# Kernel optimization log

Hardware: AMD Instinct MI355X
Metric: run time of the kernel (lower is better)

Reference implementation:

```python
import jax, jax.numpy as jnp
import numpy as np

B, S, D_IN, D_OUT, H = 2, 2048, 1024, 1024, 16
DK = D_OUT // H


def setup_inputs() -> dict:
    key = jax.random.key(0)
    ks = jax.random.split(key, 6)
    s_in = 1.0 / np.sqrt(D_IN)
    s_out = 1.0 / np.sqrt(D_OUT)
    return {
        "x": jax.random.normal(ks[0], (B, S, D_IN), dtype=jnp.float32),
        "Wq": jax.random.uniform(ks[1], (D_OUT, D_IN), jnp.float32, -s_in, s_in),
        "Wk": jax.random.uniform(ks[2], (D_OUT, D_IN), jnp.float32, -s_in, s_in),
        "Wv": jax.random.uniform(ks[3], (D_OUT, D_IN), jnp.float32, -s_in, s_in),
        "Wo": jax.random.uniform(ks[4], (D_OUT, D_OUT), jnp.float32, -s_out, s_out),
        "bo": jax.random.uniform(ks[5], (D_OUT,), jnp.float32, -s_out, s_out),
    }


def reference(x, Wq, Wk, Wv, Wo, bo):
    b, s, _ = x.shape
    # torch Linear: y = x @ W.T
    q = (x @ Wq.T).reshape(b, s, H, DK).transpose(0, 2, 1, 3)  # [b,h,s,dk]
    k = (x @ Wk.T).reshape(b, s, H, DK).transpose(0, 2, 1, 3)
    v = (x @ Wv.T).reshape(b, s, H, DK).transpose(0, 2, 1, 3)
    scores = jnp.einsum("bhqd,bhkd->bhqk", q, k)
    causal = jnp.tril(jnp.ones((s, s), dtype=bool))  # True = keep
    scores = jnp.where(causal, scores, -jnp.inf)
    attn = jax.nn.softmax(scores / np.sqrt(DK), axis=-1)
    # dropout p=0.0 (eval) -> identity
    ctx = jnp.einsum("bhqk,bhkd->bhqd", attn, v)
    ctx = ctx.transpose(0, 2, 1, 3).reshape(b, s, D_OUT)
    return ctx @ Wo.T + bo
```

## Files before the change

### kernel.cpp

```cpp
#include <hip/hip_runtime.h>
#include <stdint.h>

#define B_   2
#define S_   2048
#define DIN  1024
#define DOUT 1024
#define H_   16
#define DK_  64
#define MSZ  (B_ * S_)

typedef __bf16 bf16v8 __attribute__((ext_vector_type(8)));
typedef float  f32x4  __attribute__((ext_vector_type(4)));

__device__ __forceinline__ ushort f2b(float f) {
  union { float f; uint32_t u; } a; a.f = f;
  uint32_t u = a.u;
  u += 0x7FFFu + ((u >> 16) & 1u);
  return (ushort)(u >> 16);
}

__device__ __forceinline__ uint32_t pk2(float lo, float hi) {
  union { __bf16 h; ushort u; } a, b;
  a.h = (__bf16)lo; b.h = (__bf16)hi;
  return (uint32_t)a.u | ((uint32_t)b.u << 16);
}

#define GLDS(gp, lp) __builtin_amdgcn_global_load_lds(                         \
    (const __attribute__((address_space(1))) void*)(gp),                       \
    (__attribute__((address_space(3))) void*)(lp), 16, 0, 0)

__global__ void cvt_all(const float* __restrict__ x,  const float* __restrict__ wq,
                        const float* __restrict__ wk, const float* __restrict__ wv,
                        const float* __restrict__ wo,
                        ushort* __restrict__ xb,  ushort* __restrict__ wqb,
                        ushort* __restrict__ wkb, ushort* __restrict__ wvb,
                        ushort* __restrict__ wob) {
  int i = blockIdx.x * blockDim.x + threadIdx.x;
  const int NX = 1 << 20, NW = 1 << 18;
  const float* src; ushort* dst; int off;
  if (i < NX)               { src = x;  dst = xb;  off = i; }
  else if (i < NX + NW)     { src = wq; dst = wqb; off = i - NX; }
  else if (i < NX + 2 * NW) { src = wk; dst = wkb; off = i - NX - NW; }
  else if (i < NX + 3 * NW) { src = wv; dst = wvb; off = i - NX - 2 * NW; }
  else                      { src = wo; dst = wob; off = i - NX - 3 * NW; }
  float4 v = reinterpret_cast<const float4*>(src)[off];
  ushort4 o;
  o.x = f2b(v.x); o.y = f2b(v.y); o.z = f2b(v.z); o.w = f2b(v.w);
  reinterpret_cast<ushort4*>(dst)[off] = o;
}

__global__ __launch_bounds__(256)
void gemm_qkv(const ushort* __restrict__ A,
              const ushort* __restrict__ Bq, const ushort* __restrict__ Bk,
              const ushort* __restrict__ Bv,
              ushort* __restrict__ Oq, ushort* __restrict__ Ok,
              ushort* __restrict__ Vt, int M, int K) {
  __shared__ ushort sA[128 * 64];
  __shared__ ushort sB[128 * 64];

  const int tid  = threadIdx.x;
  const int lane = tid & 63, wid = tid >> 6;
  const int wr = wid >> 1, wc = wid & 1;
  const int g = lane >> 4, c = lane & 15;
  const int m0 = blockIdx.x * 128;

  const int wsel = blockIdx.y >> 3;
  const int n0w  = (blockIdx.y & 7) * 128;
  const ushort* Bm = (wsel == 0) ? Bq : (wsel == 1) ? Bk : Bv;

  const int msk = (c & 7) << 4;

  f32x4 acc[4][4] = {};

  for (int k0 = 0; k0 < K; k0 += 64) {
    __syncthreads();
#pragma unroll
    for (int i = 0; i < 4; ++i) {
      int idx = i * 256 + tid;
      int row = idx >> 3;
      int scol = (((idx & 7) ^ (row & 7)) << 3);
      GLDS(A  + (size_t)(m0 + row) * K + k0 + scol, (char*)sA + idx * 16);
      GLDS(Bm + (size_t)(n0w + row) * K + k0 + scol, (char*)sB + idx * 16);
    }
    __syncthreads();

    bf16v8 aF[4][2], bF[4][2];
#pragma unroll
    for (int m = 0; m < 4; ++m) {
      const char* rp = (const char*)sA + (wr * 64 + m * 16 + c) * 128;
#pragma unroll
      for (int ks = 0; ks < 2; ++ks)
        aF[m][ks] = *reinterpret_cast<const bf16v8*>(rp + ((ks * 64 + g * 16) ^ msk));
    }
#pragma unroll
    for (int n = 0; n < 4; ++n) {
      const char* rp = (const char*)sB + (wc * 64 + n * 16 + c) * 128;
#pragma unroll
      for (int ks = 0; ks < 2; ++ks)
        bF[n][ks] = *reinterpret_cast<const bf16v8*>(rp + ((ks * 64 + g * 16) ^ msk));
    }
#pragma unroll
    for (int m = 0; m < 4; ++m)
#pragma unroll
      for (int n = 0; n < 4; ++n) {
        acc[m][n] = __builtin_amdgcn_mfma_f32_16x16x32_bf16(aF[m][0], bF[n][0], acc[m][n], 0, 0, 0);
        acc[m][n] = __builtin_amdgcn_mfma_f32_16x16x32_bf16(aF[m][1], bF[n][1], acc[m][n], 0, 0, 0);
      }
  }

  __syncthreads();

  if (wsel == 2) {
#pragma unroll
    for (int m = 0; m < 4; ++m)
#pragma unroll
      for (int n = 0; n < 4; ++n) {
        int row0 = m0 + wr * 64 + g * 4 + m * 16;
        int col  = n0w + wc * 64 + c + n * 16;
        int bb = row0 >> 11, ss = row0 & 2047;
        int hh = col >> 6, dd = col & 63;
        ushort4 o4;
        o4.x = f2b(acc[m][n][0]); o4.y = f2b(acc[m][n][1]);
        o4.z = f2b(acc[m][n][2]); o4.w = f2b(acc[m][n][3]);
        *reinterpret_cast<ushort4*>(
            &Vt[((size_t)(bb * 16 + hh) * 64 + dd) * 2048 + ss]) = o4;
      }
  } else {
    const float oscale = (wsel == 0) ? 0.125f * 1.4426950408889634f : 1.0f;
    ushort* Ob = (wsel == 0) ? Oq : Ok;
    char* eb = (char*)sA + wid * 2048;
#pragma unroll
    for (int m = 0; m < 4; ++m) {
#pragma unroll
      for (int n = 0; n < 4; ++n)
#pragma unroll
        for (int i = 0; i < 4; ++i) {
          int prow = g * 4 + i;
          *(ushort*)(eb + prow * 128 + ((n * 32 + c * 2) ^ ((prow & 7) << 4))) =
              f2b(acc[m][n][i] * oscale);
        }
      const int r = lane >> 2, cq = lane & 3;
      const int m2 = (r & 7) << 4;
      bf16v8 t0 = *reinterpret_cast<const bf16v8*>(eb + r * 128 + ((cq * 32) ^ m2));
      bf16v8 t1 = *reinterpret_cast<const bf16v8*>(eb + r * 128 + ((cq * 32 + 16) ^ m2));
      ushort* Gb = Ob + (size_t)(m0 + wr * 64 + m * 16 + r) * DOUT +
                   n0w + wc * 64 + cq * 16;
      *reinterpret_cast<bf16v8*>(Gb) = t0;
      *reinterpret_cast<bf16v8*>(Gb + 8) = t1;
    }
  }
}

__global__ __launch_bounds__(512)
void gemm_proj(const ushort* __restrict__ A, const ushort* __restrict__ Bw,
               float* __restrict__ Cf, const float* __restrict__ bias,
               int M, int K) {
  __shared__ char smem[32768];

  const int tid  = threadIdx.x;
  const int lane = tid & 63, wid = tid >> 6;
  const int wr = wid >> 1, wc = wid & 1;
  const int g = lane >> 4, c = lane & 15;
  const int m0 = blockIdx.x * 128, n0 = blockIdx.y * 64;

  const int msk = (c & 7) << 4;

  f32x4 acc[2][2] = {};

  for (int k0 = 0; k0 < K; k0 += 64) {
    __syncthreads();
#pragma unroll
    for (int i = 0; i < 2; ++i) {
      int idx = i * 512 + tid;
      int row = idx >> 3;
      int scol = (((idx & 7) ^ (row & 7)) << 3);
      GLDS(A + (size_t)(m0 + row) * K + k0 + scol, smem + idx * 16);
    }
    {
      int row = tid >> 3;
      int scol = (((tid & 7) ^ (row & 7)) << 3);
      GLDS(Bw + (size_t)(n0 + row) * K + k0 + scol, smem + 16384 + tid * 16);
    }
    __syncthreads();

    bf16v8 aF[2][2], bF[2][2];
#pragma unroll
    for (int m = 0; m < 2; ++m) {
      const char* rp = smem + (wr * 32 + m * 16 + c) * 128;
#pragma unroll
      for (int ks = 0; ks < 2; ++ks)
        aF[m][ks] = *reinterpret_cast<const bf16v8*>(rp + ((ks * 64 + g * 16) ^ msk));
    }
#pragma unroll
    for (int n = 0; n < 2; ++n) {
      const char* rp = smem + 16384 + (wc * 32 + n * 16 + c) * 128;
#pragma unroll
      for (int ks = 0; ks < 2; ++ks)
        bF[n][ks] = *reinterpret_cast<const bf16v8*>(rp + ((ks * 64 + g * 16) ^ msk));
    }
#pragma unroll
    for (int m = 0; m < 2; ++m)
#pragma unroll
      for (int n = 0; n < 2; ++n) {
        acc[m][n] = __builtin_amdgcn_mfma_f32_16x16x32_bf16(aF[m][0], bF[n][0], acc[m][n], 0, 0, 0);
        acc[m][n] = __builtin_amdgcn_mfma_f32_16x16x32_bf16(aF[m][1], bF[n][1], acc[m][n], 0, 0, 0);
      }
  }

  __syncthreads();

  float bv[2];
#pragma unroll
  for (int n = 0; n < 2; ++n) bv[n] = bias[n0 + wc * 32 + n * 16 + c];

  float* ef = (float*)(smem + wid * 4096);
#pragma unroll
  for (int m = 0; m < 2; ++m)
#pragma unroll
    for (int n = 0; n < 2; ++n)
#pragma unroll
      for (int i = 0; i < 4; ++i) {
        int row = m * 16 + g * 4 + i;
        ef[row * 32 + ((n * 16 + c) ^ ((row & 7) << 2))] = acc[m][n][i] + bv[n];
      }
#pragma unroll
  for (int pass = 0; pass < 4; ++pass) {
    int idx = pass * 64 + lane;
    int row = idx >> 3, q = idx & 7;
    float4 v = *reinterpret_cast<const float4*>(
        &ef[row * 32 + ((q * 4) ^ ((row & 7) << 2))]);
    *reinterpret_cast<float4*>(
        &Cf[(size_t)(m0 + wr * 32 + row) * DOUT + n0 + wc * 32 + q * 4]) = v;
  }
}

__global__ __launch_bounds__(512)
void flash_attn(const ushort* __restrict__ Q, const ushort* __restrict__ K,
                const ushort* __restrict__ Vt, ushort* __restrict__ O) {
  __shared__ ushort sK[2][128][64];
  __shared__ ushort sV[2][2][64][64];
  __shared__ ushort sP[8][16][64];

  const int tid  = threadIdx.x;
  const int lane = tid & 63, wid = tid >> 6;
  const int wid4 = wid & 3;
  const int g = lane >> 4, c = lane & 15;

  const int orig = blockIdx.x;
  const int xcd  = orig & 7, idc = orig >> 3;
  const int bh   = xcd * 4 + (idc >> 4);
  const int tp   = idc & 15;
  const int b = bh >> 4, h = bh & 15;
  const int q0    = (wid < 4) ? tp * 64 : (31 - tp) * 64;
  const int q0max = (31 - tp) * 64;

  const ushort* Qb = Q  + (size_t)b * S_ * DOUT + h * DK_;
  const ushort* Kb = K  + (size_t)b * S_ * DOUT + h * DK_;
  const ushort* Vb = Vt + (size_t)bh * DK_ * S_;

  const int msk  = (c & 7) << 4;
  const int pswz = (c & 7) << 2;

  const int kr0 = tid >> 3,         kc0 = ((tid & 7) ^ (kr0 & 7)) << 3;
  const int kr1 = (tid + 512) >> 3, kc1 = (((tid + 512) & 7) ^ (kr1 & 7)) << 3;
  const int vd0 = (tid >> 3) & 63,  vc0 = ((tid & 7) ^ (vd0 & 7)) << 3;
  const int vh0 = tid >> 9;
  const int vd1 = ((tid + 512) >> 3) & 63;
  const int vc1 = (((tid + 512) & 7) ^ (vd1 & 7)) << 3;
  const int vh1 = (tid + 512) >> 9;

  bf16v8 qf[2];
  {
    const ushort* qrow = Qb + (size_t)(q0 + wid4 * 16 + c) * DOUT;
    qf[0] = *reinterpret_cast<const bf16v8*>(qrow + g * 8);
    qf[1] = *reinterpret_cast<const bf16v8*>(qrow + 32 + g * 8);
  }

  bf16v8 ones;
#pragma unroll
  for (int j = 0; j < 8; ++j) ones[j] = (__bf16)1.0f;

#define STAGE(BUFI, KVN)                                                       \
  {                                                                            \
    GLDS(Kb + (size_t)((KVN) + kr0) * DOUT + kc0,                              \
         (char*)&sK[BUFI][0][0] + tid * 16);                                   \
    GLDS(Kb + (size_t)((KVN) + kr1) * DOUT + kc1,                              \
         (char*)&sK[BUFI][0][0] + (tid + 512) * 16);                           \
    GLDS(Vb + (size_t)vd0 * S_ + (KVN) + vh0 * 64 + vc0,                       \
         (char*)&sV[BUFI][0][0][0] + tid * 16);                                \
    GLDS(Vb + (size_t)vd1 * S_ + (KVN) + vh1 * 64 + vc1,                       \
         (char*)&sV[BUFI][0][0][0] + (tid + 512) * 16);                        \
  }

  STAGE(0, 0);
  __syncthreads();

  f32x4 accO[4] = {};
  f32x4 accL = {};
  char* sPw = (char*)&sP[wid][0][0];
  const int qg = q0 + wid4 * 16 + c;
  const int qdiag = q0 + wid4 * 16;

  int buf = 0;
  for (int kv0 = 0; kv0 <= q0max; kv0 += 128, buf ^= 1) {
    if (kv0 + 128 <= q0max) STAGE(buf ^ 1, kv0 + 128);

#pragma unroll
    for (int sub = 0; sub < 2; ++sub) {
      const int kvs = kv0 + sub * 64;
      if (kvs <= q0) {
        const char* cK = (const char*)&sK[buf][0][0] + sub * 8192;
        const char* cV = (const char*)&sV[buf][sub][0][0];

        f32x4 s[4] = {};
        __builtin_amdgcn_s_setprio(1);
#pragma unroll
        for (int nf = 0; nf < 4; ++nf) {
          const char* rp = cK + (nf * 16 + c) * 128;
#pragma unroll
          for (int ks = 0; ks < 2; ++ks) {
            bf16v8 kf = *reinterpret_cast<const bf16v8*>(rp + ((ks * 64 + g * 16) ^ msk));
            s[nf] = __builtin_amdgcn_mfma_f32_16x16x32_bf16(kf, qf[ks], s[nf], 0, 0, 0);
          }
        }
        __builtin_amdgcn_s_setprio(0);

        if (kvs + 63 > qdiag) {
#pragma unroll
          for (int nf = 0; nf < 4; ++nf)
#pragma unroll
            for (int i = 0; i < 4; ++i)
              if (kvs + nf * 16 + g * 4 + i > qg) s[nf][i] = -1e30f;
        }

#pragma unroll
        for (int nf = 0; nf < 4; ++nf) {
          float p0 = exp2f(s[nf][0]), p1 = exp2f(s[nf][1]);
          float p2 = exp2f(s[nf][2]), p3 = exp2f(s[nf][3]);
          uint2 w2; w2.x = pk2(p0, p1); w2.y = pk2(p2, p3);
          *reinterpret_cast<uint2*>(
              sPw + c * 128 + (((nf * 8 + g * 2) ^ pswz) << 2)) = w2;
        }
        bf16v8 pf[2];
#pragma unroll
        for (int ks = 0; ks < 2; ++ks)
          pf[ks] = *reinterpret_cast<const bf16v8*>(
              sPw + c * 128 + (((ks * 16 + g * 4) ^ pswz) << 2));

        __builtin_amdgcn_s_setprio(1);
#pragma unroll
        for (int ks = 0; ks < 2; ++ks)
          accL = __builtin_amdgcn_mfma_f32_16x16x32_bf16(pf[ks], ones, accL, 0, 0, 0);
#pragma unroll
        for (int nf2 = 0; nf2 < 4; ++nf2) {
          const char* vp = cV + (nf2 * 16 + c) * 128;
#pragma unroll
          for (int ks = 0; ks < 2; ++ks) {
            bf16v8 vf = *reinterpret_cast<const bf16v8*>(vp + ((ks * 64 + g * 16) ^ msk));
            accO[nf2] = __builtin_amdgcn_mfma_f32_16x16x32_bf16(pf[ks], vf, accO[nf2], 0, 0, 0);
          }
        }
        __builtin_amdgcn_s_setprio(0);
      }
    }

    __syncthreads();
  }
#undef STAGE

#pragma unroll
  for (int nf = 0; nf < 4; ++nf)
#pragma unroll
    for (int i = 0; i < 4; ++i) {
      int prow = g * 4 + i;
      float v = accO[nf][i] / accL[i];
      *(ushort*)(sPw + prow * 128 +
                 ((nf * 32 + c * 2) ^ ((prow & 7) << 4))) = f2b(v);
    }
  {
    const int r = lane >> 2, cq = lane & 3;
    const char* base = sPw + r * 128;
    const int m2 = (r & 7) << 4;
    bf16v8 t0 = *reinterpret_cast<const bf16v8*>(base + ((cq * 32) ^ m2));
    bf16v8 t1 = *reinterpret_cast<const bf16v8*>(base + ((cq * 32 + 16) ^ m2));
    ushort* Gb = O + (size_t)b * S_ * DOUT +
                 (size_t)(q0 + wid4 * 16 + r) * DOUT + h * DK_ + cq * 16;
    *reinterpret_cast<bf16v8*>(Gb) = t0;
    *reinterpret_cast<bf16v8*>(Gb + 8) = t1;
  }
}

extern "C" void kernel_launch(void* const* d_in, const int* in_sizes, int n_in,
                              void* d_out, int out_size, void* d_ws, size_t ws_size,
                              hipStream_t stream) {
  const float* x  = (const float*)d_in[0];
  const float* Wq = (const float*)d_in[1];
  const float* Wk = (const float*)d_in[2];
  const float* Wv = (const float*)d_in[3];
  const float* Wo = (const float*)d_in[4];
  const float* bo = (const float*)d_in[5];
  float* out = (float*)d_out;

  char* ws = (char*)d_ws;
  const size_t MB = (size_t)1 << 20;
  ushort* xb  = (ushort*)(ws);
  ushort* wqb = (ushort*)(ws +  8 * MB);
  ushort* wkb = (ushort*)(ws + 10 * MB);
  ushort* wvb = (ushort*)(ws + 12 * MB);
  ushort* wob = (ushort*)(ws + 14 * MB);
  ushort* qb  = (ushort*)(ws + 16 * MB);
  ushort* kb  = (ushort*)(ws + 24 * MB);
  ushort* vtb = (ushort*)(ws + 32 * MB);
  ushort* cb  = (ushort*)(ws);

  const int ncv = (1 << 20) + 4 * (1 << 18);
  cvt_all<<<ncv / 256, 256, 0, stream>>>(x, Wq, Wk, Wv, Wo,
                                         xb, wqb, wkb, wvb, wob);

  dim3 gqkv(MSZ / 128, 24, 1);
  gemm_qkv<<<gqkv, 256, 0, stream>>>(xb, wqb, wkb, wvb, qb, kb, vtb,
                                     MSZ, DIN);

  flash_attn<<<B_ * H_ * (S_ / 128), 512, 0, stream>>>(qb, kb, vtb, cb);

  dim3 gproj(MSZ / 128, DOUT / 64, 1);
  gemm_proj<<<gproj, 512, 0, stream>>>(cb, wob, out, bo, MSZ, DOUT);
}
```

Baseline: 106.8 us.

## Enlarge QKV GEMM tiles to 256x256 with double-buffered pipelined LDS loads

```diff
diff --git a/kernel.cpp b/kernel.cpp
--- a/kernel.cpp
+++ b/kernel.cpp
@@ -49,102 +49,136 @@
   reinterpret_cast<ushort4*>(dst)[off] = o;
 }
 
-__global__ __launch_bounds__(256)
+__global__ __launch_bounds__(512)
 void gemm_qkv(const ushort* __restrict__ A,
               const ushort* __restrict__ Bq, const ushort* __restrict__ Bk,
               const ushort* __restrict__ Bv,
               ushort* __restrict__ Oq, ushort* __restrict__ Ok,
               ushort* __restrict__ Vt, int M, int K) {
-  __shared__ ushort sA[128 * 64];
-  __shared__ ushort sB[128 * 64];
+  __shared__ ushort sA[2][256][64];
+  __shared__ ushort sB[2][256][64];
 
   const int tid  = threadIdx.x;
   const int lane = tid & 63, wid = tid >> 6;
-  const int wr = wid >> 1, wc = wid & 1;
+  const int wm = wid >> 2, wn = wid & 3;
   const int g = lane >> 4, c = lane & 15;
-  const int m0 = blockIdx.x * 128;
-
-  const int wsel = blockIdx.y >> 3;
-  const int n0w  = (blockIdx.y & 7) * 128;
+  const int m0 = blockIdx.x * 256;
+
+  const int wsel = blockIdx.y >> 2;
+  const int n0w  = (blockIdx.y & 3) * 256;
   const ushort* Bm = (wsel == 0) ? Bq : (wsel == 1) ? Bk : Bv;
 
   const int msk = (c & 7) << 4;
 
-  f32x4 acc[4][4] = {};
-
-  for (int k0 = 0; k0 < K; k0 += 64) {
-    __syncthreads();
-#pragma unroll
-    for (int i = 0; i < 4; ++i) {
-      int idx = i * 256 + tid;
-      int row = idx >> 3;
-      int scol = (((idx & 7) ^ (row & 7)) << 3);
-      GLDS(A  + (size_t)(m0 + row) * K + k0 + scol, (char*)sA + idx * 16);
-      GLDS(Bm + (size_t)(n0w + row) * K + k0 + scol, (char*)sB + idx * 16);
-    }
-    __syncthreads();
-
-    bf16v8 aF[4][2], bF[4][2];
-#pragma unroll
-    for (int m = 0; m < 4; ++m) {
-      const char* rp = (const char*)sA + (wr * 64 + m * 16 + c) * 128;
-#pragma unroll
-      for (int ks = 0; ks < 2; ++ks)
-        aF[m][ks] = *reinterpret_cast<const bf16v8*>(rp + ((ks * 64 + g * 16) ^ msk));
-    }
-#pragma unroll
-    for (int n = 0; n < 4; ++n) {
-      const char* rp = (const char*)sB + (wc * 64 + n * 16 + c) * 128;
-#pragma unroll
-      for (int ks = 0; ks < 2; ++ks)
-        bF[n][ks] = *reinterpret_cast<const bf16v8*>(rp + ((ks * 64 + g * 16) ^ msk));
-    }
-#pragma unroll
-    for (int m = 0; m < 4; ++m)
-#pragma unroll
-      for (int n = 0; n < 4; ++n) {
-        acc[m][n] = __builtin_amdgcn_mfma_f32_16x16x32_bf16(aF[m][0], bF[n][0], acc[m][n], 0, 0, 0);
-        acc[m][n] = __builtin_amdgcn_mfma_f32_16x16x32_bf16(aF[m][1], bF[n][1], acc[m][n], 0, 0, 0);
-      }
-  }
-
-  __syncthreads();
+#define STAGE_A(BUF, T)                                                        \
+  { _Pragma("unroll")                                                          \
+    for (int p = 0; p < 4; ++p) {                                              \
+      int idx = p * 512 + tid; int row = idx >> 3, ch = idx & 7;               \
+      GLDS(A + (size_t)(m0 + row) * K + (T) * 64 + ((ch ^ (row & 7)) << 3),    \
+           (char*)&sA[BUF][0][0] + idx * 16);                                  \
+    } }
+#define STAGE_BH(BUF, T, H)                                                    \
+  { _Pragma("unroll")                                                          \
+    for (int p = 0; p < 2; ++p) {                                              \
+      int idx = (H) * 1024 + p * 512 + tid; int row = idx >> 3, ch = idx & 7;  \
+      GLDS(Bm + (size_t)(n0w + row) * K + (T) * 64 + ((ch ^ (row & 7)) << 3),  \
+           (char*)&sB[BUF][0][0] + idx * 16);                                  \
+    } }
+
+  f32x4 acc[8][4] = {};
+
+  STAGE_A(0, 0);
+  STAGE_BH(0, 0, 0); STAGE_BH(0, 0, 1);
+  STAGE_BH(1, 1, 0); STAGE_BH(1, 1, 1);
+  asm volatile("s_waitcnt vmcnt(4)" ::: "memory");
+  __builtin_amdgcn_s_barrier();
+  __builtin_amdgcn_sched_barrier(0);
+
+  for (int t = 0; t < 16; ++t) {
+    const int buf = t & 1;
+    const char* cA = (const char*)&sA[buf][0][0] + (wm * 128) * 128;
+    const char* cB = (const char*)&sB[buf][0][0] + (wn * 64) * 128;
+
+    bf16v8 bF[4][2];
+#pragma unroll
+    for (int nf = 0; nf < 4; ++nf) {
+      const char* rp = cB + (nf * 16 + c) * 128;
+      bF[nf][0] = *reinterpret_cast<const bf16v8*>(rp + ((g * 16) ^ msk));
+      bF[nf][1] = *reinterpret_cast<const bf16v8*>(rp + ((64 + g * 16) ^ msk));
+    }
+
+#pragma unroll
+    for (int q = 0; q < 4; ++q) {
+      bf16v8 aF[2][2];
+#pragma unroll
+      for (int mf = 0; mf < 2; ++mf) {
+        const char* rp = cA + (q * 32 + mf * 16 + c) * 128;
+        aF[mf][0] = *reinterpret_cast<const bf16v8*>(rp + ((g * 16) ^ msk));
+        aF[mf][1] = *reinterpret_cast<const bf16v8*>(rp + ((64 + g * 16) ^ msk));
+      }
+
+      if (q == 0)      { if (t + 1 < 16) STAGE_A(buf ^ 1, t + 1); }
+      else if (q == 2) { if (t + 2 < 16) STAGE_BH(buf, t + 2, 0); }
+      else if (q == 3) { if (t + 2 < 16) STAGE_BH(buf, t + 2, 1); }
+
+      __builtin_amdgcn_s_setprio(1);
+#pragma unroll
+      for (int mf = 0; mf < 2; ++mf)
+#pragma unroll
+        for (int nf = 0; nf < 4; ++nf) {
+          acc[q * 2 + mf][nf] = __builtin_amdgcn_mfma_f32_16x16x32_bf16(
+              aF[mf][0], bF[nf][0], acc[q * 2 + mf][nf], 0, 0, 0);
+          acc[q * 2 + mf][nf] = __builtin_amdgcn_mfma_f32_16x16x32_bf16(
+              aF[mf][1], bF[nf][1], acc[q * 2 + mf][nf], 0, 0, 0);
+        }
+      __builtin_amdgcn_s_setprio(0);
+
+      if (q == 3) {
+        if (t == 14)     asm volatile("s_waitcnt vmcnt(0)" ::: "memory");
+        else if (t < 14) asm volatile("s_waitcnt vmcnt(4)" ::: "memory");
+      }
+      __builtin_amdgcn_s_barrier();
+      __builtin_amdgcn_sched_barrier(0);
+    }
+  }
+#undef STAGE_A
+#undef STAGE_BH
 
   if (wsel == 2) {
 #pragma unroll
-    for (int m = 0; m < 4; ++m)
-#pragma unroll
-      for (int n = 0; n < 4; ++n) {
-        int row0 = m0 + wr * 64 + g * 4 + m * 16;
-        int col  = n0w + wc * 64 + c + n * 16;
+    for (int mf = 0; mf < 8; ++mf)
+#pragma unroll
+      for (int nf = 0; nf < 4; ++nf) {
+        int row0 = m0 + wm * 128 + mf * 16 + g * 4;
+        int col  = n0w + wn * 64 + nf * 16 + c;
         int bb = row0 >> 11, ss = row0 & 2047;
         int hh = col >> 6, dd = col & 63;
         ushort4 o4;
-        o4.x = f2b(acc[m][n][0]); o4.y = f2b(acc[m][n][1]);
-        o4.z = f2b(acc[m][n][2]); o4.w = f2b(acc[m][n][3]);
+        o4.x = f2b(acc[mf][nf][0]); o4.y = f2b(acc[mf][nf][1]);
+        o4.z = f2b(acc[mf][nf][2]); o4.w = f2b(acc[mf][nf][3]);
         *reinterpret_cast<ushort4*>(
             &Vt[((size_t)(bb * 16 + hh) * 64 + dd) * 2048 + ss]) = o4;
       }
   } else {
     const float oscale = (wsel == 0) ? 0.125f * 1.4426950408889634f : 1.0f;
     ushort* Ob = (wsel == 0) ? Oq : Ok;
-    char* eb = (char*)sA + wid * 2048;
-#pragma unroll
-    for (int m = 0; m < 4; ++m) {
-#pragma unroll
-      for (int n = 0; n < 4; ++n)
+    char* eb = (char*)&sA[0][0][0] + wid * 2048;
+#pragma unroll
+    for (int mf = 0; mf < 8; ++mf) {
+#pragma unroll
+      for (int nf = 0; nf < 4; ++nf)
 #pragma unroll
         for (int i = 0; i < 4; ++i) {
           int prow = g * 4 + i;
-          *(ushort*)(eb + prow * 128 + ((n * 32 + c * 2) ^ ((prow & 7) << 4))) =
-              f2b(acc[m][n][i] * oscale);
+          *(ushort*)(eb + prow * 128 + ((nf * 32 + c * 2) ^ ((prow & 7) << 4))) =
+              f2b(acc[mf][nf][i] * oscale);
         }
       const int r = lane >> 2, cq = lane & 3;
       const int m2 = (r & 7) << 4;
       bf16v8 t0 = *reinterpret_cast<const bf16v8*>(eb + r * 128 + ((cq * 32) ^ m2));
       bf16v8 t1 = *reinterpret_cast<const bf16v8*>(eb + r * 128 + ((cq * 32 + 16) ^ m2));
-      ushort* Gb = Ob + (size_t)(m0 + wr * 64 + m * 16 + r) * DOUT +
-                   n0w + wc * 64 + cq * 16;
+      ushort* Gb = Ob + (size_t)(m0 + wm * 128 + mf * 16 + r) * DOUT +
+                   n0w + wn * 64 + cq * 16;
       *reinterpret_cast<bf16v8*>(Gb) = t0;
       *reinterpret_cast<bf16v8*>(Gb + 8) = t1;
     }
@@ -417,8 +451,8 @@
   cvt_all<<<ncv / 256, 256, 0, stream>>>(x, Wq, Wk, Wv, Wo,
                                          xb, wqb, wkb, wvb, wob);
 
-  dim3 gqkv(MSZ / 128, 24, 1);
-  gemm_qkv<<<gqkv, 256, 0, stream>>>(xb, wqb, wkb, wvb, qb, kb, vtb,
+  dim3 gqkv(MSZ / 256, 12, 1);
+  gemm_qkv<<<gqkv, 512, 0, stream>>>(xb, wqb, wkb, wvb, qb, kb, vtb,
                                      MSZ, DIN);
 
   flash_attn<<<B_ * H_ * (S_ / 128), 512, 0, stream>>>(qb, kb, vtb, cb);
```

New measurement: 115.8 us. 1.08x slower.
